# Optimization experiments

Measured on AMD Instinct MI355X. Metric: run time of the kernel, lower is better.

## Reference

```python
import jax, jax.numpy as jnp
import numpy as np

MARGIN = 1.0
NUM_CLASSES = 64

def setup_inputs() -> dict:
    key = jax.random.key(0)
    k1, k2 = jax.random.split(key)
    embeddings = jax.random.normal(k1, (4096, 512), dtype=jnp.float32)
    labels = jax.random.randint(k2, (4096,), 0, NUM_CLASSES, dtype=jnp.int64)
    return {"embeddings": embeddings, "labels": labels}

def _pairwise_dist(x):
    # Euclidean cdist via GEMM: ||xi||^2 + ||xj||^2 - 2 xi.xj, with a
    # grad-safe sqrt (zero distance -> zero, no nan gradient).
    sq_norms = jnp.sum(x * x, axis=1)                      # [B]
    sq = sq_norms[:, None] + sq_norms[None, :] - 2.0 * (x @ x.T)
    sq = jnp.maximum(sq, 0.0)
    pos = sq > 0.0
    return jnp.where(pos, jnp.sqrt(jnp.where(pos, sq, 1.0)), 0.0)

def reference(embeddings, labels):
    B = embeddings.shape[0]
    # L2 normalize (normalize=True)
    emb = embeddings / jnp.maximum(
        jnp.linalg.norm(embeddings, axis=1, keepdims=True), 1e-12)
    dist = _pairwise_dist(emb)                             # [B, B]
    same = labels[:, None] == labels[None, :]              # [B, B]
    eye = jnp.eye(B, dtype=bool)
    pos_mask = same & ~eye
    neg_mask = ~same
    pos_cnt = jnp.sum(pos_mask, axis=1)                    # [B]
    neg_cnt = jnp.sum(neg_mask, axis=1)
    # hard_positive=False -> mean over positive distances
    pos_stat = jnp.sum(jnp.where(pos_mask, dist, 0.0), axis=1) / jnp.maximum(pos_cnt, 1)
    # hardest negative = masked min (infinity trick)
    neg_stat = jnp.min(jnp.where(neg_mask, dist, jnp.inf), axis=1)
    per_row = jnp.maximum(pos_stat - neg_stat + MARGIN, 0.0)
    valid = (pos_cnt > 0) & (neg_cnt > 0)
    n_valid = jnp.sum(valid)
    total = jnp.sum(jnp.where(valid, per_row, 0.0))
    # reduction='mean' over valid rows; 0.0 if none valid
    return jnp.where(n_valid > 0, total / jnp.maximum(n_valid, 1), 0.0)
```

## Files before the change

### kernel.cpp

```cpp
#include <hip/hip_runtime.h>
#include <hip/hip_bf16.h>

#define BSZ 4096
#define DIM 512
#define NCLS 64
#define MARGIN_F 1.0f
#define NT 32
#define NPAIR (NT * (NT + 1) / 2)
#define NBLK (NPAIR * 2)
#define NSL (2 * NT)
#define NFIN 16
#define BK 64
#define NKS (DIM / BK)

typedef float floatx4 __attribute__((ext_vector_type(4)));
typedef unsigned char u8;

#define OFF_PP  (BSZ * DIM)
#define OFF_PN  (OFF_PP + NSL * BSZ * 4)
#define OFF_ACC (OFF_PN + NSL * BSZ * 4)

__device__ __forceinline__ void gld_lds16(const u8* g, u8* l) {
    __builtin_amdgcn_global_load_lds(
        (const __attribute__((address_space(1))) unsigned int*)g,
        (__attribute__((address_space(3))) unsigned int*)l, 16, 0, 0);
}

__global__ __launch_bounds__(256) void ht_normalize(
        const float* __restrict__ emb, u8* __restrict__ ebf,
        float* __restrict__ acc_total, int* __restrict__ acc_nv,
        int* __restrict__ counter2) {
    const int lane = threadIdx.x & 63;
    const int row = blockIdx.x * 4 + (threadIdx.x >> 6);
    const float4* r4 = (const float4*)(emb + (size_t)row * DIM);
    float4 v0 = r4[lane * 2];
    float4 v1 = r4[lane * 2 + 1];
    float s = v0.x * v0.x + v0.y * v0.y + v0.z * v0.z + v0.w * v0.w
            + v1.x * v1.x + v1.y * v1.y + v1.z * v1.z + v1.w * v1.w;
#pragma unroll
    for (int off = 1; off < 64; off <<= 1) s += __shfl_xor(s, off);
    const float inv = 1.0f / fmaxf(sqrtf(s), 1e-12f);

    int d0 = 0, d1 = 0;
    d0 = __builtin_amdgcn_cvt_pk_fp8_f32(v0.x * inv, v0.y * inv, d0, 0);
    d0 = __builtin_amdgcn_cvt_pk_fp8_f32(v0.z * inv, v0.w * inv, d0, 1);
    d1 = __builtin_amdgcn_cvt_pk_fp8_f32(v1.x * inv, v1.y * inv, d1, 0);
    d1 = __builtin_amdgcn_cvt_pk_fp8_f32(v1.z * inv, v1.w * inv, d1, 1);
    uint2 o; o.x = (unsigned)d0; o.y = (unsigned)d1;
    ((uint2*)(ebf + (size_t)row * DIM))[lane] = o;

    if (blockIdx.x == 0 && threadIdx.x == 0) {
        *acc_total = 0.0f; *acc_nv = 0; *counter2 = 0;
    }
}

__global__ __launch_bounds__(256) void ht_gemm_reduce(
        const u8* __restrict__ ebf, const int* __restrict__ labels,
        float* __restrict__ part_ps, unsigned* __restrict__ part_nm) {
    __shared__ u8 sA[2][64 * BK];
    __shared__ u8 sB[2][128 * BK];
    __shared__ int sLI[64];
    __shared__ int sLJ[128];
    __shared__ float sCPps[128];
    __shared__ float sCPnm[128];

    const int p = blockIdx.x >> 1;
    const int h2 = blockIdx.x & 1;
    int rem = p, by = 0;
    while (rem >= NT - by) { rem -= NT - by; ++by; }
    const int bx = by + rem;
    const bool offd = (bx != by);

    const int t = threadIdx.x;
    const int row0 = by * 128 + h2 * 64;
    const int col0 = bx * 128;

    if (t < 64) sLI[t] = labels[row0 + t];
    else if (t < 192) sLJ[t - 64] = labels[col0 + (t - 64)];

    const int lane = t & 63;
    const int wave = t >> 6;
    const int wr = (wave >> 1) * 32;
    const int wc = (wave & 1) * 64;
    const int l15 = lane & 15;
    const int quad = lane >> 4;

    const int sa = t;
    const int ga = (sa & 3) ^ ((sa >> 3) & 3);
    const u8* gA0 = ebf + (size_t)(row0 + (sa >> 2)) * DIM + ga * 16;
    const int sb0 = t, sb1 = 256 + t;
    const int gb0 = (sb0 & 3) ^ ((sb0 >> 3) & 3);
    const int gb1 = (sb1 & 3) ^ ((sb1 >> 3) & 3);
    const u8* gB0 = ebf + (size_t)(col0 + (sb0 >> 2)) * DIM + gb0 * 16;
    const u8* gB1 = ebf + (size_t)(col0 + (sb1 >> 2)) * DIM + gb1 * 16;
    const int lbA = wave * 64 * 16;
    const int lbB0 = wave * 64 * 16;
    const int lbB1 = (256 + wave * 64) * 16;

    floatx4 acc[2][4] = {};

    gld_lds16(gA0, &sA[0][lbA]);
    gld_lds16(gB0, &sB[0][lbB0]);
    gld_lds16(gB1, &sB[0][lbB1]);

    int cur = 0;
    for (int ks = 0; ks < NKS; ++ks) {
        __syncthreads();
        if (ks + 1 < NKS) {
            const int kb = (ks + 1) * BK;
            gld_lds16(gA0 + kb, &sA[cur ^ 1][lbA]);
            gld_lds16(gB0 + kb, &sB[cur ^ 1][lbB0]);
            gld_lds16(gB1 + kb, &sB[cur ^ 1][lbB1]);
        }
#pragma unroll
        for (int h = 0; h < 2; ++h) {
            const int co = (((h * 2 + (quad >> 1)) ^ ((l15 >> 1) & 3)) * 16)
                         + (quad & 1) * 8;
            long af[2]; long bf[4];
#pragma unroll
            for (int mi = 0; mi < 2; ++mi)
                af[mi] = *(const long*)(&sA[cur][(wr + mi * 16 + l15) * BK + co]);
#pragma unroll
            for (int ni = 0; ni < 4; ++ni)
                bf[ni] = *(const long*)(&sB[cur][(wc + ni * 16 + l15) * BK + co]);
#pragma unroll
            for (int mi = 0; mi < 2; ++mi)
#pragma unroll
                for (int ni = 0; ni < 4; ++ni)
                    acc[mi][ni] = __builtin_amdgcn_mfma_f32_16x16x32_fp8_fp8(
                        af[mi], bf[ni], acc[mi][ni], 0, 0, 0);
        }
        cur ^= 1;
    }

    const float INF = __uint_as_float(0x7F800000u);
    const int rslice = 2 * bx + (wc >> 6);
    float psc[4] = {0.f, 0.f, 0.f, 0.f};
    float nmc[4] = {INF, INF, INF, INF};
#pragma unroll
    for (int mi = 0; mi < 2; ++mi) {
        const int rbase = wr + mi * 16 + quad * 4;
#pragma unroll
        for (int r = 0; r < 4; ++r) {
            const int rloc = rbase + r;
            const int gi = row0 + rloc;
            const int rl = sLI[rloc];
            float ps = 0.0f, nm = INF;
#pragma unroll
            for (int ni = 0; ni < 4; ++ni) {
                const int cloc = wc + ni * 16 + l15;
                const int gj = col0 + cloc;
                const int cl = sLJ[cloc];
                const float d = __builtin_amdgcn_sqrtf(
                    fmaxf(2.0f - 2.0f * acc[mi][ni][r], 0.0f));
                if (rl == cl) {
                    if (gi != gj) ps += d;
                    if (offd) psc[ni] += d;
                } else {
                    nm = fminf(nm, d);
                    if (offd) nmc[ni] = fminf(nmc[ni], d);
                }
            }
#pragma unroll
            for (int off = 1; off < 16; off <<= 1) {
                ps += __shfl_xor(ps, off);
                nm = fminf(nm, __shfl_xor(nm, off));
            }
            if (l15 == 0) {
                part_ps[rslice * BSZ + gi] = ps;
                part_nm[rslice * BSZ + gi] = __float_as_uint(nm);
            }
        }
    }
    if (offd) {
        const int cslice = 2 * by + h2;
        float cps[4], cnm[4];
#pragma unroll
        for (int ni = 0; ni < 4; ++ni) {
            float ps = psc[ni], nm = nmc[ni];
            ps += __shfl_xor(ps, 16); ps += __shfl_xor(ps, 32);
            nm = fminf(nm, __shfl_xor(nm, 16));
            nm = fminf(nm, __shfl_xor(nm, 32));
            cps[ni] = ps; cnm[ni] = nm;
        }
        if (wave >= 2 && quad == 0) {
#pragma unroll
            for (int ni = 0; ni < 4; ++ni) {
                const int cl = wc + ni * 16 + l15;
                sCPps[cl] = cps[ni];
                sCPnm[cl] = cnm[ni];
            }
        }
        __syncthreads();
        if (wave < 2 && quad == 0) {
#pragma unroll
            for (int ni = 0; ni < 4; ++ni) {
                const int cl = wc + ni * 16 + l15;
                const int gj = col0 + cl;
                const float ps = cps[ni] + sCPps[cl];
                const float nm = fminf(cnm[ni], sCPnm[cl]);
                part_ps[cslice * BSZ + gj] = ps;
                part_nm[cslice * BSZ + gj] = __float_as_uint(nm);
            }
        }
    }
}

__global__ __launch_bounds__(256) void ht_finalize(
        const float* __restrict__ part_ps, const unsigned* __restrict__ part_nm,
        const int* __restrict__ labels, float* __restrict__ acc_total,
        int* __restrict__ acc_nv, int* __restrict__ counter2,
        float* __restrict__ out) {
    __shared__ int hist[NCLS];
    __shared__ float sT[4];
    __shared__ int sN[4];
    const int t = threadIdx.x;
    if (t < NCLS) hist[t] = 0;
    __syncthreads();
    for (int i = t; i < BSZ; i += 256) atomicAdd(&hist[labels[i]], 1);
    __syncthreads();

    const int j = blockIdx.x * 256 + t;
    float ps = 0.0f;
    float nm = __uint_as_float(0x7F800000u);
#pragma unroll 8
    for (int s = 0; s < NSL; ++s) {
        ps += part_ps[s * BSZ + j];
        nm = fminf(nm, __uint_as_float(part_nm[s * BSZ + j]));
    }
    const int cnt = hist[labels[j]];
    const int pc = cnt - 1;
    const int nc = BSZ - cnt;
    float loss = 0.0f;
    int lv = 0;
    if (pc > 0 && nc > 0) {
        loss = fmaxf(ps / (float)pc - nm + MARGIN_F, 0.0f);
        lv = 1;
    }
#pragma unroll
    for (int off = 1; off < 64; off <<= 1) {
        loss += __shfl_xor(loss, off);
        lv += __shfl_xor(lv, off);
    }
    if ((t & 63) == 0) { sT[t >> 6] = loss; sN[t >> 6] = lv; }
    __syncthreads();
    if (t == 0) {
        const float tt = sT[0] + sT[1] + sT[2] + sT[3];
        const int nn = sN[0] + sN[1] + sN[2] + sN[3];
        __hip_atomic_fetch_add(acc_total, tt, __ATOMIC_ACQ_REL,
                               __HIP_MEMORY_SCOPE_AGENT);
        __hip_atomic_fetch_add(acc_nv, nn, __ATOMIC_ACQ_REL,
                               __HIP_MEMORY_SCOPE_AGENT);
        const int old2 = __hip_atomic_fetch_add(counter2, 1, __ATOMIC_ACQ_REL,
                                                __HIP_MEMORY_SCOPE_AGENT);
        if (old2 == NFIN - 1) {
            const float ft = __hip_atomic_load(acc_total, __ATOMIC_ACQUIRE,
                                               __HIP_MEMORY_SCOPE_AGENT);
            const int fn = __hip_atomic_load(acc_nv, __ATOMIC_ACQUIRE,
                                             __HIP_MEMORY_SCOPE_AGENT);
            out[0] = (fn > 0) ? ft / (float)fn : 0.0f;
        }
    }
}

extern "C" void kernel_launch(void* const* d_in, const int* in_sizes, int n_in,
                              void* d_out, int out_size, void* d_ws, size_t ws_size,
                              hipStream_t stream) {
    const float* emb = (const float*)d_in[0];
    const int* labels = (const int*)d_in[1];
    float* out = (float*)d_out;
    char* ws = (char*)d_ws;

    u8* ebf = (u8*)ws;
    float* part_ps = (float*)(ws + OFF_PP);
    unsigned* part_nm = (unsigned*)(ws + OFF_PN);
    float* acc_total = (float*)(ws + OFF_ACC);
    int* acc_nv = (int*)(ws + OFF_ACC + 4);
    int* counter2 = (int*)(ws + OFF_ACC + 8);

    ht_normalize<<<BSZ / 4, 256, 0, stream>>>(emb, ebf, acc_total, acc_nv,
                                              counter2);
    ht_gemm_reduce<<<NBLK, 256, 0, stream>>>(ebf, labels, part_ps, part_nm);
    ht_finalize<<<NFIN, 256, 0, stream>>>(part_ps, part_nm, labels,
                                          acc_total, acc_nv, counter2, out);
}
```

Baseline: 87.14 us.

## Fuse normalize, GEMM-reduce and finalize into one persistent kernel with grid barriers

Merges the three kernel launches into a single kernel of 1024 blocks. Blocks first normalize rows, meet at a spin-wait grid barrier on an atomic counter, then loop over the 1056 GEMM tiles. The last 16 blocks to finish take a ticket and run the finalize step after waiting for all blocks. This removes launch gaps between stages but relies on all 1024 blocks being co-resident, adds a memset and barrier spin costs, and leaves the GEMM tile loop imbalanced, since 32 blocks do two tiles.

```diff
diff --git a/kernel.cpp b/kernel.cpp
--- a/kernel.cpp
+++ b/kernel.cpp
@@ -12,6 +12,7 @@
 #define NFIN 16
 #define BK 64
 #define NKS (DIM / BK)
+#define GRID 1024
 
 typedef float floatx4 __attribute__((ext_vector_type(4)));
 typedef unsigned char u8;
@@ -26,201 +27,223 @@
         (__attribute__((address_space(3))) unsigned int*)l, 16, 0, 0);
 }
 
-__global__ __launch_bounds__(256) void ht_normalize(
-        const float* __restrict__ emb, u8* __restrict__ ebf,
-        float* __restrict__ acc_total, int* __restrict__ acc_nv,
-        int* __restrict__ counter2) {
-    const int lane = threadIdx.x & 63;
-    const int row = blockIdx.x * 4 + (threadIdx.x >> 6);
-    const float4* r4 = (const float4*)(emb + (size_t)row * DIM);
-    float4 v0 = r4[lane * 2];
-    float4 v1 = r4[lane * 2 + 1];
-    float s = v0.x * v0.x + v0.y * v0.y + v0.z * v0.z + v0.w * v0.w
-            + v1.x * v1.x + v1.y * v1.y + v1.z * v1.z + v1.w * v1.w;
-#pragma unroll
-    for (int off = 1; off < 64; off <<= 1) s += __shfl_xor(s, off);
-    const float inv = 1.0f / fmaxf(sqrtf(s), 1e-12f);
-
-    int d0 = 0, d1 = 0;
-    d0 = __builtin_amdgcn_cvt_pk_fp8_f32(v0.x * inv, v0.y * inv, d0, 0);
-    d0 = __builtin_amdgcn_cvt_pk_fp8_f32(v0.z * inv, v0.w * inv, d0, 1);
-    d1 = __builtin_amdgcn_cvt_pk_fp8_f32(v1.x * inv, v1.y * inv, d1, 0);
-    d1 = __builtin_amdgcn_cvt_pk_fp8_f32(v1.z * inv, v1.w * inv, d1, 1);
-    uint2 o; o.x = (unsigned)d0; o.y = (unsigned)d1;
-    ((uint2*)(ebf + (size_t)row * DIM))[lane] = o;
-
-    if (blockIdx.x == 0 && threadIdx.x == 0) {
-        *acc_total = 0.0f; *acc_nv = 0; *counter2 = 0;
-    }
-}
-
-__global__ __launch_bounds__(256) void ht_gemm_reduce(
-        const u8* __restrict__ ebf, const int* __restrict__ labels,
-        float* __restrict__ part_ps, unsigned* __restrict__ part_nm) {
+__global__ __launch_bounds__(256, 4) void ht_fused(
+        const float* __restrict__ emb, const int* __restrict__ labels,
+        u8* __restrict__ ebf, float* __restrict__ part_ps,
+        unsigned* __restrict__ part_nm, float* __restrict__ acc_total,
+        int* __restrict__ acc_nv, int* __restrict__ counter2,
+        int* __restrict__ norm_done, int* __restrict__ gemm_done,
+        float* __restrict__ out) {
     __shared__ u8 sA[2][64 * BK];
     __shared__ u8 sB[2][128 * BK];
     __shared__ int sLI[64];
     __shared__ int sLJ[128];
     __shared__ float sCPps[128];
     __shared__ float sCPnm[128];
-
-    const int p = blockIdx.x >> 1;
-    const int h2 = blockIdx.x & 1;
-    int rem = p, by = 0;
-    while (rem >= NT - by) { rem -= NT - by; ++by; }
-    const int bx = by + rem;
-    const bool offd = (bx != by);
+    __shared__ int sTicket;
+    __shared__ int hist[NCLS];
+    __shared__ float sT[4];
+    __shared__ int sN[4];
 
     const int t = threadIdx.x;
-    const int row0 = by * 128 + h2 * 64;
-    const int col0 = bx * 128;
-
-    if (t < 64) sLI[t] = labels[row0 + t];
-    else if (t < 192) sLJ[t - 64] = labels[col0 + (t - 64)];
-
     const int lane = t & 63;
     const int wave = t >> 6;
+
+    {
+        const int row = blockIdx.x * 4 + wave;
+        const float4* r4 = (const float4*)(emb + (size_t)row * DIM);
+        float4 v0 = r4[lane * 2];
+        float4 v1 = r4[lane * 2 + 1];
+        float s = v0.x * v0.x + v0.y * v0.y + v0.z * v0.z + v0.w * v0.w
+                + v1.x * v1.x + v1.y * v1.y + v1.z * v1.z + v1.w * v1.w;
+#pragma unroll
+        for (int off = 1; off < 64; off <<= 1) s += __shfl_xor(s, off);
+        const float inv = 1.0f / fmaxf(sqrtf(s), 1e-12f);
+
+        int d0 = 0, d1 = 0;
+        d0 = __builtin_amdgcn_cvt_pk_fp8_f32(v0.x * inv, v0.y * inv, d0, 0);
+        d0 = __builtin_amdgcn_cvt_pk_fp8_f32(v0.z * inv, v0.w * inv, d0, 1);
+        d1 = __builtin_amdgcn_cvt_pk_fp8_f32(v1.x * inv, v1.y * inv, d1, 0);
+        d1 = __builtin_amdgcn_cvt_pk_fp8_f32(v1.z * inv, v1.w * inv, d1, 1);
+        uint2 o; o.x = (unsigned)d0; o.y = (unsigned)d1;
+        ((uint2*)(ebf + (size_t)row * DIM))[lane] = o;
+    }
+
+    __threadfence();
+    __syncthreads();
+    if (t == 0) {
+        __hip_atomic_fetch_add(norm_done, 1, __ATOMIC_ACQ_REL,
+                               __HIP_MEMORY_SCOPE_AGENT);
+        while (__hip_atomic_load(norm_done, __ATOMIC_ACQUIRE,
+                                 __HIP_MEMORY_SCOPE_AGENT) < GRID)
+            __builtin_amdgcn_s_sleep(8);
+    }
+    __syncthreads();
+
     const int wr = (wave >> 1) * 32;
     const int wc = (wave & 1) * 64;
     const int l15 = lane & 15;
     const int quad = lane >> 4;
 
-    const int sa = t;
-    const int ga = (sa & 3) ^ ((sa >> 3) & 3);
-    const u8* gA0 = ebf + (size_t)(row0 + (sa >> 2)) * DIM + ga * 16;
-    const int sb0 = t, sb1 = 256 + t;
-    const int gb0 = (sb0 & 3) ^ ((sb0 >> 3) & 3);
-    const int gb1 = (sb1 & 3) ^ ((sb1 >> 3) & 3);
-    const u8* gB0 = ebf + (size_t)(col0 + (sb0 >> 2)) * DIM + gb0 * 16;
-    const u8* gB1 = ebf + (size_t)(col0 + (sb1 >> 2)) * DIM + gb1 * 16;
-    const int lbA = wave * 64 * 16;
-    const int lbB0 = wave * 64 * 16;
-    const int lbB1 = (256 + wave * 64) * 16;
-
-    floatx4 acc[2][4] = {};
-
-    gld_lds16(gA0, &sA[0][lbA]);
-    gld_lds16(gB0, &sB[0][lbB0]);
-    gld_lds16(gB1, &sB[0][lbB1]);
-
-    int cur = 0;
-    for (int ks = 0; ks < NKS; ++ks) {
+    for (int tb = blockIdx.x; tb < NBLK; tb += GRID) {
         __syncthreads();
-        if (ks + 1 < NKS) {
-            const int kb = (ks + 1) * BK;
-            gld_lds16(gA0 + kb, &sA[cur ^ 1][lbA]);
-            gld_lds16(gB0 + kb, &sB[cur ^ 1][lbB0]);
-            gld_lds16(gB1 + kb, &sB[cur ^ 1][lbB1]);
+
+        const int p = tb >> 1;
+        const int h2 = tb & 1;
+        int rem = p, by = 0;
+        while (rem >= NT - by) { rem -= NT - by; ++by; }
+        const int bx = by + rem;
+        const bool offd = (bx != by);
+
+        const int row0 = by * 128 + h2 * 64;
+        const int col0 = bx * 128;
+
+        if (t < 64) sLI[t] = labels[row0 + t];
+        else if (t < 192) sLJ[t - 64] = labels[col0 + (t - 64)];
+
+        const int sa = t;
+        const int ga = (sa & 3) ^ ((sa >> 3) & 3);
+        const u8* gA0 = ebf + (size_t)(row0 + (sa >> 2)) * DIM + ga * 16;
+        const int sb0 = t, sb1 = 256 + t;
+        const int gb0 = (sb0 & 3) ^ ((sb0 >> 3) & 3);
+        const int gb1 = (sb1 & 3) ^ ((sb1 >> 3) & 3);
+        const u8* gB0 = ebf + (size_t)(col0 + (sb0 >> 2)) * DIM + gb0 * 16;
+        const u8* gB1 = ebf + (size_t)(col0 + (sb1 >> 2)) * DIM + gb1 * 16;
+        const int lbA = wave * 64 * 16;
+        const int lbB0 = wave * 64 * 16;
+        const int lbB1 = (256 + wave * 64) * 16;
+
+        floatx4 acc[2][4] = {};
+
+        gld_lds16(gA0, &sA[0][lbA]);
+        gld_lds16(gB0, &sB[0][lbB0]);
+        gld_lds16(gB1, &sB[0][lbB1]);
+
+        int cur = 0;
+        for (int ks = 0; ks < NKS; ++ks) {
+            __syncthreads();
+            if (ks + 1 < NKS) {
+                const int kb = (ks + 1) * BK;
+                gld_lds16(gA0 + kb, &sA[cur ^ 1][lbA]);
+                gld_lds16(gB0 + kb, &sB[cur ^ 1][lbB0]);
+                gld_lds16(gB1 + kb, &sB[cur ^ 1][lbB1]);
+            }
+#pragma unroll
+            for (int h = 0; h < 2; ++h) {
+                const int co = (((h * 2 + (quad >> 1)) ^ ((l15 >> 1) & 3)) * 16)
+                             + (quad & 1) * 8;
+                long af[2]; long bf[4];
+#pragma unroll
+                for (int mi = 0; mi < 2; ++mi)
+                    af[mi] = *(const long*)(&sA[cur][(wr + mi * 16 + l15) * BK + co]);
+#pragma unroll
+                for (int ni = 0; ni < 4; ++ni)
+                    bf[ni] = *(const long*)(&sB[cur][(wc + ni * 16 + l15) * BK + co]);
+#pragma unroll
+                for (int mi = 0; mi < 2; ++mi)
+#pragma unroll
+                    for (int ni = 0; ni < 4; ++ni)
+                        acc[mi][ni] = __builtin_amdgcn_mfma_f32_16x16x32_fp8_fp8(
+                            af[mi], bf[ni], acc[mi][ni], 0, 0, 0);
+            }
+            cur ^= 1;
         }
-#pragma unroll
-        for (int h = 0; h < 2; ++h) {
-            const int co = (((h * 2 + (quad >> 1)) ^ ((l15 >> 1) & 3)) * 16)
-                         + (quad & 1) * 8;
-            long af[2]; long bf[4];
-#pragma unroll
-            for (int mi = 0; mi < 2; ++mi)
-                af[mi] = *(const long*)(&sA[cur][(wr + mi * 16 + l15) * BK + co]);
-#pragma unroll
-            for (int ni = 0; ni < 4; ++ni)
-                bf[ni] = *(const long*)(&sB[cur][(wc + ni * 16 + l15) * BK + co]);
-#pragma unroll
-            for (int mi = 0; mi < 2; ++mi)
-#pragma unroll
-                for (int ni = 0; ni < 4; ++ni)
-                    acc[mi][ni] = __builtin_amdgcn_mfma_f32_16x16x32_fp8_fp8(
-                        af[mi], bf[ni], acc[mi][ni], 0, 0, 0);
+
+        const float INF = __uint_as_float(0x7F800000u);
+        const int rslice = 2 * bx + (wc >> 6);
+        float psc[4] = {0.f, 0.f, 0.f, 0.f};
+        float nmc[4] = {INF, INF, INF, INF};
+#pragma unroll
+        for (int mi = 0; mi < 2; ++mi) {
+            const int rbase = wr + mi * 16 + quad * 4;
+#pragma unroll
+            for (int r = 0; r < 4; ++r) {
+                const int rloc = rbase + r;
+                const int gi = row0 + rloc;
+                const int rl = sLI[rloc];
+                float ps = 0.0f, nm = INF;
+#pragma unroll
+                for (int ni = 0; ni < 4; ++ni) {
+                    const int cloc = wc + ni * 16 + l15;
+                    const int gj = col0 + cloc;
+                    const int cl = sLJ[cloc];
+                    const float d = __builtin_amdgcn_sqrtf(
+                        fmaxf(2.0f - 2.0f * acc[mi][ni][r], 0.0f));
+                    if (rl == cl) {
+                        if (gi != gj) ps += d;
+                        if (offd) psc[ni] += d;
+                    } else {
+                        nm = fminf(nm, d);
+                        if (offd) nmc[ni] = fminf(nmc[ni], d);
+                    }
+                }
+#pragma unroll
+                for (int off = 1; off < 16; off <<= 1) {
+                    ps += __shfl_xor(ps, off);
+                    nm = fminf(nm, __shfl_xor(nm, off));
+                }
+                if (l15 == 0) {
+                    part_ps[rslice * BSZ + gi] = ps;
+                    part_nm[rslice * BSZ + gi] = __float_as_uint(nm);
+                }
+            }
         }
-        cur ^= 1;
-    }
-
-    const float INF = __uint_as_float(0x7F800000u);
-    const int rslice = 2 * bx + (wc >> 6);
-    float psc[4] = {0.f, 0.f, 0.f, 0.f};
-    float nmc[4] = {INF, INF, INF, INF};
-#pragma unroll
-    for (int mi = 0; mi < 2; ++mi) {
-        const int rbase = wr + mi * 16 + quad * 4;
-#pragma unroll
-        for (int r = 0; r < 4; ++r) {
-            const int rloc = rbase + r;
-            const int gi = row0 + rloc;
-            const int rl = sLI[rloc];
-            float ps = 0.0f, nm = INF;
+        if (offd) {
+            const int cslice = 2 * by + h2;
+            float cps[4], cnm[4];
 #pragma unroll
             for (int ni = 0; ni < 4; ++ni) {
-                const int cloc = wc + ni * 16 + l15;
-                const int gj = col0 + cloc;
-                const int cl = sLJ[cloc];
-                const float d = __builtin_amdgcn_sqrtf(
-                    fmaxf(2.0f - 2.0f * acc[mi][ni][r], 0.0f));
-                if (rl == cl) {
-                    if (gi != gj) ps += d;
-                    if (offd) psc[ni] += d;
-                } else {
-                    nm = fminf(nm, d);
-                    if (offd) nmc[ni] = fminf(nmc[ni], d);
-                }
-            }
-#pragma unroll
-            for (int off = 1; off < 16; off <<= 1) {
-                ps += __shfl_xor(ps, off);
-                nm = fminf(nm, __shfl_xor(nm, off));
-            }
-            if (l15 == 0) {
-                part_ps[rslice * BSZ + gi] = ps;
-                part_nm[rslice * BSZ + gi] = __float_as_uint(nm);
+                float ps = psc[ni], nm = nmc[ni];
+                ps += __shfl_xor(ps, 16); ps += __shfl_xor(ps, 32);
+                nm = fminf(nm, __shfl_xor(nm, 16));
+                nm = fminf(nm, __shfl_xor(nm, 32));
+                cps[ni] = ps; cnm[ni] = nm;
+            }
+            if (wave >= 2 && quad == 0) {
+#pragma unroll
+                for (int ni = 0; ni < 4; ++ni) {
+                    const int cl = wc + ni * 16 + l15;
+                    sCPps[cl] = cps[ni];
+                    sCPnm[cl] = cnm[ni];
+                }
+            }
+            __syncthreads();
+            if (wave < 2 && quad == 0) {
+#pragma unroll
+                for (int ni = 0; ni < 4; ++ni) {
+                    const int cl = wc + ni * 16 + l15;
+                    const int gj = col0 + cl;
+                    const float ps = cps[ni] + sCPps[cl];
+                    const float nm = fminf(cnm[ni], sCPnm[cl]);
+                    part_ps[cslice * BSZ + gj] = ps;
+                    part_nm[cslice * BSZ + gj] = __float_as_uint(nm);
+                }
             }
         }
     }
-    if (offd) {
-        const int cslice = 2 * by + h2;
-        float cps[4], cnm[4];
-#pragma unroll
-        for (int ni = 0; ni < 4; ++ni) {
-            float ps = psc[ni], nm = nmc[ni];
-            ps += __shfl_xor(ps, 16); ps += __shfl_xor(ps, 32);
-            nm = fminf(nm, __shfl_xor(nm, 16));
-            nm = fminf(nm, __shfl_xor(nm, 32));
-            cps[ni] = ps; cnm[ni] = nm;
-        }
-        if (wave >= 2 && quad == 0) {
-#pragma unroll
-            for (int ni = 0; ni < 4; ++ni) {
-                const int cl = wc + ni * 16 + l15;
-                sCPps[cl] = cps[ni];
-                sCPnm[cl] = cnm[ni];
-            }
-        }
-        __syncthreads();
-        if (wave < 2 && quad == 0) {
-#pragma unroll
-            for (int ni = 0; ni < 4; ++ni) {
-                const int cl = wc + ni * 16 + l15;
-                const int gj = col0 + cl;
-                const float ps = cps[ni] + sCPps[cl];
-                const float nm = fminf(cnm[ni], sCPnm[cl]);
-                part_ps[cslice * BSZ + gj] = ps;
-                part_nm[cslice * BSZ + gj] = __float_as_uint(nm);
-            }
-        }
-    }
-}
-
-__global__ __launch_bounds__(256) void ht_finalize(
-        const float* __restrict__ part_ps, const unsigned* __restrict__ part_nm,
-        const int* __restrict__ labels, float* __restrict__ acc_total,
-        int* __restrict__ acc_nv, int* __restrict__ counter2,
-        float* __restrict__ out) {
-    __shared__ int hist[NCLS];
-    __shared__ float sT[4];
-    __shared__ int sN[4];
-    const int t = threadIdx.x;
+
+    __threadfence();
+    __syncthreads();
+    if (t == 0)
+        sTicket = __hip_atomic_fetch_add(gemm_done, 1, __ATOMIC_ACQ_REL,
+                                         __HIP_MEMORY_SCOPE_AGENT);
+    __syncthreads();
+    const int ticket = sTicket;
+    if (ticket < GRID - NFIN) return;
+    if (t == 0) {
+        while (__hip_atomic_load(gemm_done, __ATOMIC_ACQUIRE,
+                                 __HIP_MEMORY_SCOPE_AGENT) < GRID)
+            __builtin_amdgcn_s_sleep(8);
+    }
+    __syncthreads();
+
+    const int chunk = ticket - (GRID - NFIN);
     if (t < NCLS) hist[t] = 0;
     __syncthreads();
     for (int i = t; i < BSZ; i += 256) atomicAdd(&hist[labels[i]], 1);
     __syncthreads();
 
-    const int j = blockIdx.x * 256 + t;
+    const int j = chunk * 256 + t;
     float ps = 0.0f;
     float nm = __uint_as_float(0x7F800000u);
 #pragma unroll 8
@@ -277,10 +300,11 @@
     float* acc_total = (float*)(ws + OFF_ACC);
     int* acc_nv = (int*)(ws + OFF_ACC + 4);
     int* counter2 = (int*)(ws + OFF_ACC + 8);
-
-    ht_normalize<<<BSZ / 4, 256, 0, stream>>>(emb, ebf, acc_total, acc_nv,
-                                              counter2);
-    ht_gemm_reduce<<<NBLK, 256, 0, stream>>>(ebf, labels, part_ps, part_nm);
-    ht_finalize<<<NFIN, 256, 0, stream>>>(part_ps, part_nm, labels,
-                                          acc_total, acc_nv, counter2, out);
+    int* norm_done = (int*)(ws + OFF_ACC + 12);
+    int* gemm_done = (int*)(ws + OFF_ACC + 16);
+
+    hipMemsetAsync(ws + OFF_ACC, 0, 32, stream);
+    ht_fused<<<GRID, 256, 0, stream>>>(emb, labels, ebf, part_ps, part_nm,
+                                       acc_total, acc_nv, counter2,
+                                       norm_done, gemm_done, out);
 }
```

Result: slower. 295.4 us (+239.0%).

## Use full 128x128 output tile per block, dropping half-tile split and LDS column merge

Applied to the files above, without the earlier changes.

Each GEMM block now computes a full 128x128 tile of the upper-triangular pair grid instead of two 64x128 halves. Each wave takes a 64x64 subtile with 4x4 MFMA accumulators, so more compute is done per LDS load and per global A/B load. Each wave writes column partials directly into its own slice, which removes the shared-memory merge and the extra barrier. The cost is half as many blocks (528 instead of 1056), more registers per thread with a launch bound of 4, and double the A buffer in LDS.

```diff
diff --git a/kernel.cpp b/kernel.cpp
--- a/kernel.cpp
+++ b/kernel.cpp
@@ -7,7 +7,6 @@
 #define MARGIN_F 1.0f
 #define NT 32
 #define NPAIR (NT * (NT + 1) / 2)
-#define NBLK (NPAIR * 2)
 #define NSL (2 * NT)
 #define NFIN 16
 #define BK 64
@@ -54,77 +53,72 @@
     }
 }
 
-__global__ __launch_bounds__(256) void ht_gemm_reduce(
+__global__ __launch_bounds__(256, 4) void ht_gemm_reduce(
         const u8* __restrict__ ebf, const int* __restrict__ labels,
         float* __restrict__ part_ps, unsigned* __restrict__ part_nm) {
-    __shared__ u8 sA[2][64 * BK];
+    __shared__ u8 sA[2][128 * BK];
     __shared__ u8 sB[2][128 * BK];
-    __shared__ int sLI[64];
+    __shared__ int sLI[128];
     __shared__ int sLJ[128];
-    __shared__ float sCPps[128];
-    __shared__ float sCPnm[128];
-
-    const int p = blockIdx.x >> 1;
-    const int h2 = blockIdx.x & 1;
+
+    const int p = blockIdx.x;
     int rem = p, by = 0;
     while (rem >= NT - by) { rem -= NT - by; ++by; }
     const int bx = by + rem;
     const bool offd = (bx != by);
 
     const int t = threadIdx.x;
-    const int row0 = by * 128 + h2 * 64;
+    const int row0 = by * 128;
     const int col0 = bx * 128;
 
-    if (t < 64) sLI[t] = labels[row0 + t];
-    else if (t < 192) sLJ[t - 64] = labels[col0 + (t - 64)];
+    if (t < 128) sLI[t] = labels[row0 + t];
+    else sLJ[t - 128] = labels[col0 + (t - 128)];
 
     const int lane = t & 63;
     const int wave = t >> 6;
-    const int wr = (wave >> 1) * 32;
+    const int wr = (wave >> 1) * 64;
     const int wc = (wave & 1) * 64;
     const int l15 = lane & 15;
     const int quad = lane >> 4;
 
-    const int sa = t;
-    const int ga = (sa & 3) ^ ((sa >> 3) & 3);
-    const u8* gA0 = ebf + (size_t)(row0 + (sa >> 2)) * DIM + ga * 16;
-    const int sb0 = t, sb1 = 256 + t;
-    const int gb0 = (sb0 & 3) ^ ((sb0 >> 3) & 3);
-    const int gb1 = (sb1 & 3) ^ ((sb1 >> 3) & 3);
-    const u8* gB0 = ebf + (size_t)(col0 + (sb0 >> 2)) * DIM + gb0 * 16;
-    const u8* gB1 = ebf + (size_t)(col0 + (sb1 >> 2)) * DIM + gb1 * 16;
-    const int lbA = wave * 64 * 16;
-    const int lbB0 = wave * 64 * 16;
-    const int lbB1 = (256 + wave * 64) * 16;
-
-    floatx4 acc[2][4] = {};
-
-    gld_lds16(gA0, &sA[0][lbA]);
-    gld_lds16(gB0, &sB[0][lbB0]);
-    gld_lds16(gB1, &sB[0][lbB1]);
+    const int gc = (t & 3) ^ ((t >> 3) & 3);
+    const u8* gA0 = ebf + (size_t)(row0 + (t >> 2)) * DIM + gc * 16;
+    const u8* gA1 = ebf + (size_t)(row0 + 64 + (t >> 2)) * DIM + gc * 16;
+    const u8* gB0 = ebf + (size_t)(col0 + (t >> 2)) * DIM + gc * 16;
+    const u8* gB1 = ebf + (size_t)(col0 + 64 + (t >> 2)) * DIM + gc * 16;
+    const int lb0 = wave * 64 * 16;
+    const int lb1 = (256 + wave * 64) * 16;
+
+    floatx4 acc[4][4] = {};
+
+    gld_lds16(gA0, &sA[0][lb0]);
+    gld_lds16(gA1, &sA[0][lb1]);
+    gld_lds16(gB0, &sB[0][lb0]);
+    gld_lds16(gB1, &sB[0][lb1]);
 
     int cur = 0;
     for (int ks = 0; ks < NKS; ++ks) {
         __syncthreads();
         if (ks + 1 < NKS) {
             const int kb = (ks + 1) * BK;
-            gld_lds16(gA0 + kb, &sA[cur ^ 1][lbA]);
-            gld_lds16(gB0 + kb, &sB[cur ^ 1][lbB0]);
-            gld_lds16(gB1 + kb, &sB[cur ^ 1][lbB1]);
+            gld_lds16(gA0 + kb, &sA[cur ^ 1][lb0]);
+            gld_lds16(gA1 + kb, &sA[cur ^ 1][lb1]);
+            gld_lds16(gB0 + kb, &sB[cur ^ 1][lb0]);
+            gld_lds16(gB1 + kb, &sB[cur ^ 1][lb1]);
         }
 #pragma unroll
         for (int h = 0; h < 2; ++h) {
             const int co = (((h * 2 + (quad >> 1)) ^ ((l15 >> 1) & 3)) * 16)
                          + (quad & 1) * 8;
-            long af[2]; long bf[4];
-#pragma unroll
-            for (int mi = 0; mi < 2; ++mi)
+            long af[4]; long bf[4];
+#pragma unroll
+            for (int mi = 0; mi < 4; ++mi)
                 af[mi] = *(const long*)(&sA[cur][(wr + mi * 16 + l15) * BK + co]);
 #pragma unroll
             for (int ni = 0; ni < 4; ++ni)
                 bf[ni] = *(const long*)(&sB[cur][(wc + ni * 16 + l15) * BK + co]);
 #pragma unroll
-            for (int mi = 0; mi < 2; ++mi)
+            for (int mi = 0; mi < 4; ++mi)
 #pragma unroll
                 for (int ni = 0; ni < 4; ++ni)
                     acc[mi][ni] = __builtin_amdgcn_mfma_f32_16x16x32_fp8_fp8(
@@ -138,7 +132,7 @@
     float psc[4] = {0.f, 0.f, 0.f, 0.f};
     float nmc[4] = {INF, INF, INF, INF};
 #pragma unroll
-    for (int mi = 0; mi < 2; ++mi) {
+    for (int mi = 0; mi < 4; ++mi) {
         const int rbase = wr + mi * 16 + quad * 4;
 #pragma unroll
         for (int r = 0; r < 4; ++r) {
@@ -173,32 +167,15 @@
         }
     }
     if (offd) {
-        const int cslice = 2 * by + h2;
-        float cps[4], cnm[4];
+        const int cslice = 2 * by + (wr >> 6);
 #pragma unroll
         for (int ni = 0; ni < 4; ++ni) {
             float ps = psc[ni], nm = nmc[ni];
             ps += __shfl_xor(ps, 16); ps += __shfl_xor(ps, 32);
             nm = fminf(nm, __shfl_xor(nm, 16));
             nm = fminf(nm, __shfl_xor(nm, 32));
-            cps[ni] = ps; cnm[ni] = nm;
-        }
-        if (wave >= 2 && quad == 0) {
-#pragma unroll
-            for (int ni = 0; ni < 4; ++ni) {
-                const int cl = wc + ni * 16 + l15;
-                sCPps[cl] = cps[ni];
-                sCPnm[cl] = cnm[ni];
-            }
-        }
-        __syncthreads();
-        if (wave < 2 && quad == 0) {
-#pragma unroll
-            for (int ni = 0; ni < 4; ++ni) {
-                const int cl = wc + ni * 16 + l15;
-                const int gj = col0 + cl;
-                const float ps = cps[ni] + sCPps[cl];
-                const float nm = fminf(cnm[ni], sCPnm[cl]);
+            if (quad == 0) {
+                const int gj = col0 + wc + ni * 16 + l15;
                 part_ps[cslice * BSZ + gj] = ps;
                 part_nm[cslice * BSZ + gj] = __float_as_uint(nm);
             }
@@ -278,9 +255,9 @@
     int* acc_nv = (int*)(ws + OFF_ACC + 4);
     int* counter2 = (int*)(ws + OFF_ACC + 8);
 
-    ht_normalize<<<BSZ / 4, 256, 0, stream>>>(emb, ebf, acc_total, acc_nv,
-                                              counter2);
-    ht_gemm_reduce<<<NBLK, 256, 0, stream>>>(ebf, labels, part_ps, part_nm);
+    ht_normalize<<<BSZ / 4, 256, 0, stream>>>(emb, labels ? ebf : ebf, acc_total,
+                                              acc_nv, counter2);
+    ht_gemm_reduce<<<NPAIR, 256, 0, stream>>>(ebf, labels, part_ps, part_nm);
     ht_finalize<<<NFIN, 256, 0, stream>>>(part_ps, part_nm, labels,
                                           acc_total, acc_nv, counter2, out);
 }
```

Result: no change. 88.71 us (+1.8%).
